# Performance work log

Hardware: AMD Instinct MI355X
Metric: run time of the kernel (lower is better)

Reference implementation:

```python
import jax, jax.numpy as jnp
import numpy as np

CHUNK = 1024  # rows of pc0 processed per tile to avoid materializing the full NxM matrix


def _min_sqdist(a, b):
    """For each row of a [N,3], min squared distance to rows of b [M,3]."""
    b_sq = jnp.sum(b * b, axis=1)  # [M]

    def tile_min(ac):  # ac: [CHUNK, 3]
        d = jnp.sum(ac * ac, axis=1)[:, None] + b_sq[None, :] - 2.0 * (ac @ b.T)
        return jnp.min(d, axis=1)

    n, dim = a.shape
    return jax.lax.map(tile_min, a.reshape(n // CHUNK, CHUNK, dim)).reshape(n)


def setup_inputs() -> dict:
    key = jax.random.key(0)
    k0, k1 = jax.random.split(key)
    pc0 = jax.random.normal(k0, (65536, 3), dtype=jnp.float32)
    pc1 = jax.random.normal(k1, (65536, 3), dtype=jnp.float32)
    return {"pc0": pc0, "pc1": pc1}


def reference(pc0, pc1):
    # chamfer forward: dist0[i] = min_j ||pc0[i]-pc1[j]||^2
    dist0 = _min_sqdist(pc0, pc1)
    mask = dist0 <= 2.0
    # mean over selected elements (boolean mask is constant wrt grads, as in torch)
    return jnp.sum(jnp.where(mask, dist0, 0.0)) / jnp.sum(mask).astype(dist0.dtype)
```

## Files before the change

kernel.cpp:

```cpp
#include <hip/hip_runtime.h>


constexpr int   NPTS  = 65536;
constexpr int   G     = 64;
constexpr int   NC    = G * G * G;
constexpr float H     = 0.125f;
constexpr float ORG   = -4.0f;
constexpr float INVH  = 8.0f;
constexpr int   BLOCK = 256;
constexpr int   PBLOCKS = 256;
constexpr int   SB    = 128;
constexpr int   CHUNK = NC / SB;

__device__ __forceinline__ int cellOf(float x) {
  int c = (int)floorf((x - ORG) * INVH);
  return min(max(c, 0), G - 1);
}

__global__ __launch_bounds__(BLOCK) void count_kernel(
    const float* __restrict__ pc0, const float* __restrict__ pc1,
    unsigned* __restrict__ counts0, unsigned* __restrict__ counts1) {
  const int gid = blockIdx.x * BLOCK + threadIdx.x;
  const float* p; unsigned* cnt; int i;
  if (gid < NPTS) { p = pc1; cnt = counts1; i = gid; }
  else            { p = pc0; cnt = counts0; i = gid - NPTS; }
  const float x = p[3 * i], y = p[3 * i + 1], z = p[3 * i + 2];
  const int cid = (cellOf(z) * G + cellOf(y)) * G + cellOf(x);
  atomicAdd(&cnt[cid], 1u);
}

__global__ __launch_bounds__(1024) void scan_partial_kernel(
    const unsigned* __restrict__ counts0, const unsigned* __restrict__ counts1,
    unsigned* __restrict__ partials) {
  const unsigned* counts = blockIdx.y ? counts0 : counts1;
  const int base = blockIdx.x * CHUNK + threadIdx.x * 2;
  unsigned sum = counts[base] + counts[base + 1];
  for (int o = 32; o; o >>= 1) sum += __shfl_down(sum, o, 64);
  __shared__ unsigned ws[16];
  if ((threadIdx.x & 63) == 0) ws[threadIdx.x >> 6] = sum;
  __syncthreads();
  if (threadIdx.x == 0) {
    unsigned t = 0;
    for (int w = 0; w < 16; ++w) t += ws[w];
    partials[blockIdx.y * SB + blockIdx.x] = t;
  }
}

__global__ __launch_bounds__(256) void scan_mid_kernel(
    unsigned* __restrict__ partials) {
  const int tid = threadIdx.x;
  const int g   = tid >> 7;
  const int li  = tid & 127;
  const unsigned v = partials[g * SB + li];
  unsigned inc = v;
  for (int o = 1; o < 64; o <<= 1) {
    const unsigned t = __shfl_up(inc, o, 64);
    if ((tid & 63) >= o) inc += t;
  }
  __shared__ unsigned wt[4];
  if ((tid & 63) == 63) wt[tid >> 6] = inc;
  __syncthreads();
  const unsigned woff = ((tid >> 6) & 1) ? wt[g << 1] : 0u;
  partials[g * SB + li] = woff + inc - v;
}

__global__ __launch_bounds__(1024) void scan_final_kernel(
    const unsigned* __restrict__ counts0, unsigned* __restrict__ cur0,
    const unsigned* __restrict__ counts1, unsigned* __restrict__ cur1,
    const unsigned* __restrict__ partials) {
  const unsigned* counts = blockIdx.y ? counts0 : counts1;
  unsigned* cur          = blockIdx.y ? cur0    : cur1;
  const int tid = threadIdx.x;
  const int base = blockIdx.x * CHUNK + tid * 2;
  const unsigned a = counts[base], b = counts[base + 1];
  const unsigned tsum = a + b;
  unsigned inc = tsum;
  for (int o = 1; o < 64; o <<= 1) {
    const unsigned t = __shfl_up(inc, o, 64);
    if ((tid & 63) >= o) inc += t;
  }
  __shared__ unsigned wt[16];
  if ((tid & 63) == 63) wt[tid >> 6] = inc;
  __syncthreads();
  if (tid < 16) {
    unsigned w = wt[tid];
    for (int o = 1; o < 16; o <<= 1) {
      const unsigned t = __shfl_up(w, o, 16);
      if (tid >= o) w += t;
    }
    wt[tid] = w;
  }
  __syncthreads();
  const unsigned woff = (tid >> 6) ? wt[(tid >> 6) - 1] : 0u;
  const unsigned off =
      partials[blockIdx.y * SB + blockIdx.x] + woff + inc - tsum;
  cur[base] = off;
  cur[base + 1] = off + a;
}

__global__ __launch_bounds__(BLOCK) void scatter_kernel(
    const float* __restrict__ pc0, const float* __restrict__ pc1,
    unsigned* __restrict__ cur0, unsigned* __restrict__ cur1,
    float4* __restrict__ q, float4* __restrict__ s) {
  const int gid = blockIdx.x * BLOCK + threadIdx.x;
  const float* p; unsigned* cur; float4* dst; int i;
  if (gid < NPTS) { p = pc1; cur = cur1; dst = s; i = gid; }
  else            { p = pc0; cur = cur0; dst = q; i = gid - NPTS; }
  const float x = p[3 * i], y = p[3 * i + 1], z = p[3 * i + 2];
  const int cid = (cellOf(z) * G + cellOf(y)) * G + cellOf(x);
  const unsigned pos = atomicAdd(&cur[cid], 1u);
  dst[pos] = make_float4(x, y, z, 0.f);
}

__global__ __launch_bounds__(BLOCK) void query_kernel(
    const float4* __restrict__ q, const unsigned* __restrict__ ends,
    const float4* __restrict__ s,
    unsigned* __restrict__ wl, float* __restrict__ wlBest,
    unsigned* __restrict__ pendCnt, float* __restrict__ bkt) {
  const int i = blockIdx.x * BLOCK + threadIdx.x;
  const float4 p = q[i];
  const int cx = cellOf(p.x), cy = cellOf(p.y), cz = cellOf(p.z);
  const int x0 = max(cx - 1, 0), x1 = min(cx + 1, G - 1);

  unsigned rs[9], re[9];
#pragma unroll
  for (int rr = 0; rr < 9; ++rr) {
    const int zz = cz + rr / 3 - 1, yy = cy + rr % 3 - 1;
    const bool ok = (zz >= 0) && (zz < G) && (yy >= 0) && (yy < G);
    const int rb = ok ? (zz * G + yy) * G : 0;
    rs[rr] = ok ? ((rb + x0) ? ends[rb + x0 - 1] : 0u) : 0u;
    re[rr] = ok ? ends[rb + x1] : 0u;
  }
  float best = 3.4e38f;
#pragma unroll
  for (int rr = 0; rr < 9; ++rr) {
#pragma unroll 4
    for (unsigned j = rs[rr]; j < re[rr]; ++j) {
      const float4 c = s[j];
      const float dx = p.x - c.x, dy = p.y - c.y, dz = p.z - c.z;
      best = fminf(best, fmaf(dx, dx, fmaf(dy, dy, dz * dz)));
    }
  }

  float v = 0.f, c = 0.f;
  if (best > H * H) {
    const unsigned k = atomicAdd(pendCnt, 1u);
    wl[k] = (unsigned)i; wlBest[k] = best;
  } else if (best <= 2.0f) { v = best; c = 1.0f; }

  for (int o = 32; o; o >>= 1) {
    v += __shfl_down(v, o, 64);
    c += __shfl_down(c, o, 64);
  }
  __shared__ float wsum[BLOCK / 64], wcnt[BLOCK / 64];
  const int wid = threadIdx.x >> 6;
  if ((threadIdx.x & 63) == 0) { wsum[wid] = v; wcnt[wid] = c; }
  __syncthreads();
  if (threadIdx.x == 0) {
    float bv = 0.f, bc = 0.f;
    for (int w = 0; w < BLOCK / 64; ++w) { bv += wsum[w]; bc += wcnt[w]; }
    if (bc != 0.f) {
      atomicAdd(&bkt[2 * (blockIdx.x & 63) + 0], bv);
      atomicAdd(&bkt[2 * (blockIdx.x & 63) + 1], bc);
    }
  }
}

__global__ __launch_bounds__(BLOCK) void pending_kernel(
    const float4* __restrict__ q, const unsigned* __restrict__ ends,
    const float4* __restrict__ s,
    const unsigned* __restrict__ wl, const float* __restrict__ wlBest,
    unsigned* __restrict__ pendCnt, float* __restrict__ bkt,
    unsigned* __restrict__ done, float* __restrict__ out) {
  __shared__ int snP;
  __shared__ float wsum[BLOCK / 64], wcnt[BLOCK / 64];
  __shared__ int isLast;
  __shared__ float fs[BLOCK / 64], fc[BLOCK / 64];
  if (threadIdx.x == 0) snP = (int)atomicAdd(pendCnt, 0u);
  __syncthreads();
  const int lane = threadIdx.x & 63, wid = threadIdx.x >> 6;
  const int gw = blockIdx.x * (BLOCK / 64) + wid;
  const int nW = PBLOCKS * (BLOCK / 64);
  float v = 0.f, c = 0.f;

  for (int it = gw; it < snP; it += nW) {
    const unsigned qi = wl[it];
    const float4 p = q[qi];
    const int cx = cellOf(p.x), cy = cellOf(p.y), cz = cellOf(p.z);
    float best = wlBest[it];

    for (int r = 2; r <= G; ++r) {
      const float cov = H * (float)(r - 1);
      if (best <= cov * cov) break;
      if (best > 2.0f && cov * cov >= 2.0f) break;
      const int S = 8 * r + 2 * (2 * r - 1) * (2 * r - 1);
      float b = best;
      for (int sI = lane; sI < S; sI += 64) {
        int dz, dy, xa, xb;
        if (sI < 8 * r) {
          if (sI < 2 * r + 1)      { dz = -r; dy = sI - r; }
          else if (sI < 4 * r + 2) { dz =  r; dy = sI - (2 * r + 1) - r; }
          else { const int t2 = sI - (4 * r + 2); dz = (t2 >> 1) - (r - 1);
                 dy = (t2 & 1) ? r : -r; }
          xa = cx - r; xb = cx + r;
        } else {
          const int t2 = sI - 8 * r, ci = t2 >> 1, w1 = 2 * r - 1;
          dz = ci / w1 - (r - 1); dy = ci % w1 - (r - 1);
          xa = xb = (t2 & 1) ? cx + r : cx - r;
        }
        const int zz = cz + dz, yy = cy + dy;
        if (zz < 0 || zz >= G || yy < 0 || yy >= G) continue;
        const int a = max(xa, 0), e = min(xb, G - 1);
        if (a > e) continue;
        const int rb = (zz * G + yy) * G;
        const unsigned js = (rb + a) ? ends[rb + a - 1] : 0u;
        const unsigned je = ends[rb + e];
        for (unsigned j = js; j < je; ++j) {
          const float4 cd = s[j];
          const float dx = p.x - cd.x, dyv = p.y - cd.y, dzv = p.z - cd.z;
          b = fminf(b, fmaf(dx, dx, fmaf(dyv, dyv, dzv * dzv)));
        }
      }
      for (int o = 32; o; o >>= 1) b = fminf(b, __shfl_xor(b, o, 64));
      best = b;
    }
    if (lane == 0 && best <= 2.0f) { v += best; c += 1.0f; }
  }

  if (lane == 0) { wsum[wid] = v; wcnt[wid] = c; }
  __syncthreads();
  if (threadIdx.x == 0) {
    float bv = 0.f, bc = 0.f;
    for (int w = 0; w < BLOCK / 64; ++w) { bv += wsum[w]; bc += wcnt[w]; }
    if (bc != 0.f) {
      atomicAdd(&bkt[2 * (blockIdx.x & 63) + 0], bv);
      atomicAdd(&bkt[2 * (blockIdx.x & 63) + 1], bc);
    }
    __threadfence();
    isLast = (atomicAdd(done, 1u) == (unsigned)(PBLOCKS - 1));
  }
  __syncthreads();
  if (isLast) {
    const float val = (threadIdx.x < 128) ? atomicAdd(&bkt[threadIdx.x], 0.0f) : 0.0f;
    float sv = (threadIdx.x & 1) ? 0.f : val;
    float cv = (threadIdx.x & 1) ? val : 0.f;
    for (int o = 32; o; o >>= 1) {
      sv += __shfl_down(sv, o, 64);
      cv += __shfl_down(cv, o, 64);
    }
    if (lane == 0) { fs[wid] = sv; fc[wid] = cv; }
    __syncthreads();
    if (threadIdx.x == 0) {
      float S = 0.f, C = 0.f;
      for (int w = 0; w < BLOCK / 64; ++w) { S += fs[w]; C += fc[w]; }
      out[0] = S / C;
    }
  }
}

extern "C" void kernel_launch(void* const* d_in, const int* in_sizes, int n_in,
                              void* d_out, int out_size, void* d_ws, size_t ws_size,
                              hipStream_t stream) {
  const float* pc0 = (const float*)d_in[0];
  const float* pc1 = (const float*)d_in[1];
  float* out = (float*)d_out;

  char* w = (char*)d_ws;
  auto nxt = [&](size_t bytes) {
    char* p = w; w += (bytes + 255) & ~(size_t)255; return p;
  };
  unsigned* counts1  = (unsigned*)nxt((size_t)NC * 4);
  unsigned* counts0  = (unsigned*)nxt((size_t)NC * 4);
  char*     misc     = nxt(1024);
  float*    bkt      = (float*)misc;
  unsigned* done     = (unsigned*)(misc + 512);
  unsigned* pendCnt  = (unsigned*)(misc + 516);
  unsigned* partials = (unsigned*)nxt((size_t)2 * SB * 4);
  unsigned* cur1     = (unsigned*)nxt((size_t)NC * 4);
  unsigned* cur0     = (unsigned*)nxt((size_t)NC * 4);
  float4*   s        = (float4*)nxt((size_t)NPTS * 16);
  float4*   q        = (float4*)nxt((size_t)NPTS * 16);
  unsigned* wl       = (unsigned*)nxt((size_t)NPTS * 4);
  float*    wlBest   = (float*)nxt((size_t)NPTS * 4);

  hipMemsetAsync(counts1, 0, (size_t)2 * NC * 4 + 1024, stream);

  count_kernel<<<2 * NPTS / BLOCK, BLOCK, 0, stream>>>(pc0, pc1, counts0, counts1);
  scan_partial_kernel<<<dim3(SB, 2), 1024, 0, stream>>>(counts0, counts1, partials);
  scan_mid_kernel<<<1, 256, 0, stream>>>(partials);
  scan_final_kernel<<<dim3(SB, 2), 1024, 0, stream>>>(counts0, cur0,
                                                      counts1, cur1, partials);
  scatter_kernel<<<2 * NPTS / BLOCK, BLOCK, 0, stream>>>(
      pc0, pc1, cur0, cur1, q, s);
  query_kernel<<<NPTS / BLOCK, BLOCK, 0, stream>>>(q, cur1, s, wl, wlBest,
                                                   pendCnt, bkt);
  pending_kernel<<<PBLOCKS, BLOCK, 0, stream>>>(q, cur1, s, wl, wlBest,
                                                pendCnt, bkt, done, out);
}
```

Before: 157.0 us.

## Add coarse 16^3 grid for pending-query ring search

Builds a second, coarser uniform grid (cell size 0.5) over pc1 alongside the fine 64^3 grid. Its counts, prefix scan and scatter are folded into the existing count, scan_mid and scatter kernels. The pending_kernel, which handles queries not resolved by the fine 3x3x3 search, now expands rings over the coarse grid (at most 4 rings) instead of many fine rings. This cuts per-query ring iterations and end-offset lookups for far queries, at the cost of an extra atomic scatter, 1 MB more workspace, and a larger single-block scan.

```diff
diff --git a/kernel.cpp b/kernel.cpp
--- a/kernel.cpp
+++ b/kernel.cpp
@@ -7,6 +7,10 @@
 constexpr float H     = 0.125f;
 constexpr float ORG   = -4.0f;
 constexpr float INVH  = 8.0f;
+constexpr int   G2    = 16;
+constexpr int   NC2   = G2 * G2 * G2;
+constexpr float H2    = 0.5f;
+constexpr float INVH2 = 2.0f;
 constexpr int   BLOCK = 256;
 constexpr int   PBLOCKS = 256;
 constexpr int   SB    = 128;
@@ -16,17 +20,25 @@
   int c = (int)floorf((x - ORG) * INVH);
   return min(max(c, 0), G - 1);
 }
+__device__ __forceinline__ int cellOf2(float x) {
+  int c = (int)floorf((x - ORG) * INVH2);
+  return min(max(c, 0), G2 - 1);
+}
 
 __global__ __launch_bounds__(BLOCK) void count_kernel(
     const float* __restrict__ pc0, const float* __restrict__ pc1,
-    unsigned* __restrict__ counts0, unsigned* __restrict__ counts1) {
+    unsigned* __restrict__ counts0, unsigned* __restrict__ counts1,
+    unsigned* __restrict__ counts2) {
   const int gid = blockIdx.x * BLOCK + threadIdx.x;
-  const float* p; unsigned* cnt; int i;
-  if (gid < NPTS) { p = pc1; cnt = counts1; i = gid; }
-  else            { p = pc0; cnt = counts0; i = gid - NPTS; }
-  const float x = p[3 * i], y = p[3 * i + 1], z = p[3 * i + 2];
-  const int cid = (cellOf(z) * G + cellOf(y)) * G + cellOf(x);
-  atomicAdd(&cnt[cid], 1u);
+  if (gid < NPTS) {
+    const float x = pc1[3 * gid], y = pc1[3 * gid + 1], z = pc1[3 * gid + 2];
+    atomicAdd(&counts1[(cellOf(z) * G + cellOf(y)) * G + cellOf(x)], 1u);
+    atomicAdd(&counts2[(cellOf2(z) * G2 + cellOf2(y)) * G2 + cellOf2(x)], 1u);
+  } else {
+    const int i = gid - NPTS;
+    const float x = pc0[3 * i], y = pc0[3 * i + 1], z = pc0[3 * i + 2];
+    atomicAdd(&counts0[(cellOf(z) * G + cellOf(y)) * G + cellOf(x)], 1u);
+  }
 }
 
 __global__ __launch_bounds__(1024) void scan_partial_kernel(
@@ -46,22 +58,52 @@
   }
 }
 
-__global__ __launch_bounds__(256) void scan_mid_kernel(
-    unsigned* __restrict__ partials) {
+__global__ __launch_bounds__(1024) void scan_mid_kernel(
+    unsigned* __restrict__ partials,
+    const unsigned* __restrict__ counts2, unsigned* __restrict__ cur2) {
+  __shared__ unsigned wt[4];
+  __shared__ unsigned wt2[16];
   const int tid = threadIdx.x;
-  const int g   = tid >> 7;
-  const int li  = tid & 127;
-  const unsigned v = partials[g * SB + li];
-  unsigned inc = v;
+  unsigned v = 0, inc = 0; int g = 0, li = 0;
+  if (tid < 256) {
+    g = tid >> 7; li = tid & 127;
+    v = partials[g * SB + li];
+    inc = v;
+    for (int o = 1; o < 64; o <<= 1) {
+      const unsigned t = __shfl_up(inc, o, 64);
+      if ((tid & 63) >= o) inc += t;
+    }
+    if ((tid & 63) == 63) wt[tid >> 6] = inc;
+  }
+  __syncthreads();
+  if (tid < 256) {
+    const unsigned woff = ((tid >> 6) & 1) ? wt[g << 1] : 0u;
+    partials[g * SB + li] = woff + inc - v;
+  }
+  const int base = tid * 4;
+  const unsigned c0 = counts2[base], c1 = counts2[base + 1],
+                 c2 = counts2[base + 2], c3 = counts2[base + 3];
+  const unsigned run = c0 + c1 + c2 + c3;
+  unsigned inc2 = run;
   for (int o = 1; o < 64; o <<= 1) {
-    const unsigned t = __shfl_up(inc, o, 64);
-    if ((tid & 63) >= o) inc += t;
-  }
-  __shared__ unsigned wt[4];
-  if ((tid & 63) == 63) wt[tid >> 6] = inc;
-  __syncthreads();
-  const unsigned woff = ((tid >> 6) & 1) ? wt[g << 1] : 0u;
-  partials[g * SB + li] = woff + inc - v;
+    const unsigned t = __shfl_up(inc2, o, 64);
+    if ((tid & 63) >= o) inc2 += t;
+  }
+  if ((tid & 63) == 63) wt2[tid >> 6] = inc2;
+  __syncthreads();
+  if (tid < 16) {
+    unsigned w = wt2[tid];
+    for (int o = 1; o < 16; o <<= 1) {
+      const unsigned t = __shfl_up(w, o, 16);
+      if (tid >= o) w += t;
+    }
+    wt2[tid] = w;
+  }
+  __syncthreads();
+  const unsigned woff2 = (tid >> 6) ? wt2[(tid >> 6) - 1] : 0u;
+  unsigned r = woff2 + inc2 - run;
+  cur2[base] = r; cur2[base + 1] = r + c0;
+  cur2[base + 2] = r + c0 + c1; cur2[base + 3] = r + c0 + c1 + c2;
 }
 
 __global__ __launch_bounds__(1024) void scan_final_kernel(
@@ -101,15 +143,22 @@
 __global__ __launch_bounds__(BLOCK) void scatter_kernel(
     const float* __restrict__ pc0, const float* __restrict__ pc1,
     unsigned* __restrict__ cur0, unsigned* __restrict__ cur1,
-    float4* __restrict__ q, float4* __restrict__ s) {
+    unsigned* __restrict__ cur2,
+    float4* __restrict__ q, float4* __restrict__ s, float4* __restrict__ s2) {
   const int gid = blockIdx.x * BLOCK + threadIdx.x;
-  const float* p; unsigned* cur; float4* dst; int i;
-  if (gid < NPTS) { p = pc1; cur = cur1; dst = s; i = gid; }
-  else            { p = pc0; cur = cur0; dst = q; i = gid - NPTS; }
-  const float x = p[3 * i], y = p[3 * i + 1], z = p[3 * i + 2];
-  const int cid = (cellOf(z) * G + cellOf(y)) * G + cellOf(x);
-  const unsigned pos = atomicAdd(&cur[cid], 1u);
-  dst[pos] = make_float4(x, y, z, 0.f);
+  if (gid < NPTS) {
+    const float x = pc1[3 * gid], y = pc1[3 * gid + 1], z = pc1[3 * gid + 2];
+    const float4 pt = make_float4(x, y, z, 0.f);
+    const int cid  = (cellOf(z) * G + cellOf(y)) * G + cellOf(x);
+    const int cid2 = (cellOf2(z) * G2 + cellOf2(y)) * G2 + cellOf2(x);
+    s[atomicAdd(&cur1[cid], 1u)] = pt;
+    s2[atomicAdd(&cur2[cid2], 1u)] = pt;
+  } else {
+    const int i = gid - NPTS;
+    const float x = pc0[3 * i], y = pc0[3 * i + 1], z = pc0[3 * i + 2];
+    const int cid = (cellOf(z) * G + cellOf(y)) * G + cellOf(x);
+    q[atomicAdd(&cur0[cid], 1u)] = make_float4(x, y, z, 0.f);
+  }
 }
 
 __global__ __launch_bounds__(BLOCK) void query_kernel(
@@ -167,8 +216,8 @@
 }
 
 __global__ __launch_bounds__(BLOCK) void pending_kernel(
-    const float4* __restrict__ q, const unsigned* __restrict__ ends,
-    const float4* __restrict__ s,
+    const float4* __restrict__ q,
+    const unsigned* __restrict__ ends2, const float4* __restrict__ s2,
     const unsigned* __restrict__ wl, const float* __restrict__ wlBest,
     unsigned* __restrict__ pendCnt, float* __restrict__ bkt,
     unsigned* __restrict__ done, float* __restrict__ out) {
@@ -186,18 +235,20 @@
   for (int it = gw; it < snP; it += nW) {
     const unsigned qi = wl[it];
     const float4 p = q[qi];
-    const int cx = cellOf(p.x), cy = cellOf(p.y), cz = cellOf(p.z);
+    const int cx = cellOf2(p.x), cy = cellOf2(p.y), cz = cellOf2(p.z);
     float best = wlBest[it];
 
-    for (int r = 2; r <= G; ++r) {
-      const float cov = H * (float)(r - 1);
+    for (int r = 1; r <= 4; ++r) {
+      const float cov = H2 * (float)(r - 1);
       if (best <= cov * cov) break;
       if (best > 2.0f && cov * cov >= 2.0f) break;
-      const int S = 8 * r + 2 * (2 * r - 1) * (2 * r - 1);
+      const int S = (r == 1) ? 9 : 8 * r + 2 * (2 * r - 1) * (2 * r - 1);
       float b = best;
       for (int sI = lane; sI < S; sI += 64) {
         int dz, dy, xa, xb;
-        if (sI < 8 * r) {
+        if (r == 1) {
+          dz = sI / 3 - 1; dy = sI % 3 - 1; xa = cx - 1; xb = cx + 1;
+        } else if (sI < 8 * r) {
           if (sI < 2 * r + 1)      { dz = -r; dy = sI - r; }
           else if (sI < 4 * r + 2) { dz =  r; dy = sI - (2 * r + 1) - r; }
           else { const int t2 = sI - (4 * r + 2); dz = (t2 >> 1) - (r - 1);
@@ -209,14 +260,14 @@
           xa = xb = (t2 & 1) ? cx + r : cx - r;
         }
         const int zz = cz + dz, yy = cy + dy;
-        if (zz < 0 || zz >= G || yy < 0 || yy >= G) continue;
-        const int a = max(xa, 0), e = min(xb, G - 1);
+        if (zz < 0 || zz >= G2 || yy < 0 || yy >= G2) continue;
+        const int a = max(xa, 0), e = min(xb, G2 - 1);
         if (a > e) continue;
-        const int rb = (zz * G + yy) * G;
-        const unsigned js = (rb + a) ? ends[rb + a - 1] : 0u;
-        const unsigned je = ends[rb + e];
+        const int rb = (zz * G2 + yy) * G2;
+        const unsigned js = (rb + a) ? ends2[rb + a - 1] : 0u;
+        const unsigned je = ends2[rb + e];
         for (unsigned j = js; j < je; ++j) {
-          const float4 cd = s[j];
+          const float4 cd = s2[j];
           const float dx = p.x - cd.x, dyv = p.y - cd.y, dzv = p.z - cd.z;
           b = fminf(b, fmaf(dx, dx, fmaf(dyv, dyv, dzv * dzv)));
         }
@@ -271,6 +322,7 @@
   };
   unsigned* counts1  = (unsigned*)nxt((size_t)NC * 4);
   unsigned* counts0  = (unsigned*)nxt((size_t)NC * 4);
+  unsigned* counts2  = (unsigned*)nxt((size_t)NC2 * 4);
   char*     misc     = nxt(1024);
   float*    bkt      = (float*)misc;
   unsigned* done     = (unsigned*)(misc + 512);
@@ -278,22 +330,25 @@
   unsigned* partials = (unsigned*)nxt((size_t)2 * SB * 4);
   unsigned* cur1     = (unsigned*)nxt((size_t)NC * 4);
   unsigned* cur0     = (unsigned*)nxt((size_t)NC * 4);
+  unsigned* cur2     = (unsigned*)nxt((size_t)NC2 * 4);
   float4*   s        = (float4*)nxt((size_t)NPTS * 16);
+  float4*   s2       = (float4*)nxt((size_t)NPTS * 16);
   float4*   q        = (float4*)nxt((size_t)NPTS * 16);
   unsigned* wl       = (unsigned*)nxt((size_t)NPTS * 4);
   float*    wlBest   = (float*)nxt((size_t)NPTS * 4);
 
-  hipMemsetAsync(counts1, 0, (size_t)2 * NC * 4 + 1024, stream);
-
-  count_kernel<<<2 * NPTS / BLOCK, BLOCK, 0, stream>>>(pc0, pc1, counts0, counts1);
+  hipMemsetAsync(counts1, 0, (size_t)2 * NC * 4 + (size_t)NC2 * 4 + 1024, stream);
+
+  count_kernel<<<2 * NPTS / BLOCK, BLOCK, 0, stream>>>(pc0, pc1,
+                                                       counts0, counts1, counts2);
   scan_partial_kernel<<<dim3(SB, 2), 1024, 0, stream>>>(counts0, counts1, partials);
-  scan_mid_kernel<<<1, 256, 0, stream>>>(partials);
+  scan_mid_kernel<<<1, 1024, 0, stream>>>(partials, counts2, cur2);
   scan_final_kernel<<<dim3(SB, 2), 1024, 0, stream>>>(counts0, cur0,
                                                       counts1, cur1, partials);
   scatter_kernel<<<2 * NPTS / BLOCK, BLOCK, 0, stream>>>(
-      pc0, pc1, cur0, cur1, q, s);
+      pc0, pc1, cur0, cur1, cur2, q, s, s2);
   query_kernel<<<NPTS / BLOCK, BLOCK, 0, stream>>>(q, cur1, s, wl, wlBest,
                                                    pendCnt, bkt);
-  pending_kernel<<<PBLOCKS, BLOCK, 0, stream>>>(q, cur1, s, wl, wlBest,
+  pending_kernel<<<PBLOCKS, BLOCK, 0, stream>>>(q, cur2, s2, wl, wlBest,
                                                 pendCnt, bkt, done, out);
 }
```

Measured after the change: 311.1 us. 98.1% more time.

## Split query scan across thread pairs and use coarser shells in pending search

Applied to the files above, without the earlier changes.

The query kernel now gives two threads to each query point. Each thread scans alternating candidates in the 3x3x3 neighbourhood, and the pair merges its minimum with a lane shuffle, which doubles the thread count to spread the per-point work. The pending kernel now expands shells over a coarser 32^3 virtual grid built from 2x2 blocks of fine cells. This needs fewer shell iterations and wave reductions per far point, but scans more candidates per shell. Halving useful lanes in the reduction path and the coarser shells may cost extra work in exchange.

```diff
diff --git a/kernel.cpp b/kernel.cpp
--- a/kernel.cpp
+++ b/kernel.cpp
@@ -7,6 +7,9 @@
 constexpr float H     = 0.125f;
 constexpr float ORG   = -4.0f;
 constexpr float INVH  = 8.0f;
+constexpr int   G3    = 32;
+constexpr float H3    = 0.25f;
+constexpr float INVH3 = 4.0f;
 constexpr int   BLOCK = 256;
 constexpr int   PBLOCKS = 256;
 constexpr int   SB    = 128;
@@ -15,6 +18,10 @@
 __device__ __forceinline__ int cellOf(float x) {
   int c = (int)floorf((x - ORG) * INVH);
   return min(max(c, 0), G - 1);
+}
+__device__ __forceinline__ int cellOf3(float x) {
+  int c = (int)floorf((x - ORG) * INVH3);
+  return min(max(c, 0), G3 - 1);
 }
 
 __global__ __launch_bounds__(BLOCK) void count_kernel(
@@ -25,8 +32,7 @@
   if (gid < NPTS) { p = pc1; cnt = counts1; i = gid; }
   else            { p = pc0; cnt = counts0; i = gid - NPTS; }
   const float x = p[3 * i], y = p[3 * i + 1], z = p[3 * i + 2];
-  const int cid = (cellOf(z) * G + cellOf(y)) * G + cellOf(x);
-  atomicAdd(&cnt[cid], 1u);
+  atomicAdd(&cnt[(cellOf(z) * G + cellOf(y)) * G + cellOf(x)], 1u);
 }
 
 __global__ __launch_bounds__(1024) void scan_partial_kernel(
@@ -108,8 +114,7 @@
   else            { p = pc0; cur = cur0; dst = q; i = gid - NPTS; }
   const float x = p[3 * i], y = p[3 * i + 1], z = p[3 * i + 2];
   const int cid = (cellOf(z) * G + cellOf(y)) * G + cellOf(x);
-  const unsigned pos = atomicAdd(&cur[cid], 1u);
-  dst[pos] = make_float4(x, y, z, 0.f);
+  dst[atomicAdd(&cur[cid], 1u)] = make_float4(x, y, z, 0.f);
 }
 
 __global__ __launch_bounds__(BLOCK) void query_kernel(
@@ -117,7 +122,9 @@
     const float4* __restrict__ s,
     unsigned* __restrict__ wl, float* __restrict__ wlBest,
     unsigned* __restrict__ pendCnt, float* __restrict__ bkt) {
-  const int i = blockIdx.x * BLOCK + threadIdx.x;
+  const int gtid = blockIdx.x * BLOCK + threadIdx.x;
+  const int i   = gtid >> 1;
+  const int sub = gtid & 1;
   const float4 p = q[i];
   const int cx = cellOf(p.x), cy = cellOf(p.y), cz = cellOf(p.z);
   const int x0 = max(cx - 1, 0), x1 = min(cx + 1, G - 1);
@@ -135,18 +142,21 @@
 #pragma unroll
   for (int rr = 0; rr < 9; ++rr) {
 #pragma unroll 4
-    for (unsigned j = rs[rr]; j < re[rr]; ++j) {
+    for (unsigned j = rs[rr] + sub; j < re[rr]; j += 2) {
       const float4 c = s[j];
       const float dx = p.x - c.x, dy = p.y - c.y, dz = p.z - c.z;
       best = fminf(best, fmaf(dx, dx, fmaf(dy, dy, dz * dz)));
     }
   }
+  best = fminf(best, __shfl_xor(best, 1, 64));
 
   float v = 0.f, c = 0.f;
-  if (best > H * H) {
-    const unsigned k = atomicAdd(pendCnt, 1u);
-    wl[k] = (unsigned)i; wlBest[k] = best;
-  } else if (best <= 2.0f) { v = best; c = 1.0f; }
+  if (sub == 0) {
+    if (best > H * H) {
+      const unsigned k = atomicAdd(pendCnt, 1u);
+      wl[k] = (unsigned)i; wlBest[k] = best;
+    } else if (best <= 2.0f) { v = best; c = 1.0f; }
+  }
 
   for (int o = 32; o; o >>= 1) {
     v += __shfl_down(v, o, 64);
@@ -167,8 +177,8 @@
 }
 
 __global__ __launch_bounds__(BLOCK) void pending_kernel(
-    const float4* __restrict__ q, const unsigned* __restrict__ ends,
-    const float4* __restrict__ s,
+    const float4* __restrict__ q,
+    const unsigned* __restrict__ ends, const float4* __restrict__ s,
     const unsigned* __restrict__ wl, const float* __restrict__ wlBest,
     unsigned* __restrict__ pendCnt, float* __restrict__ bkt,
     unsigned* __restrict__ done, float* __restrict__ out) {
@@ -186,18 +196,20 @@
   for (int it = gw; it < snP; it += nW) {
     const unsigned qi = wl[it];
     const float4 p = q[qi];
-    const int cx = cellOf(p.x), cy = cellOf(p.y), cz = cellOf(p.z);
+    const int cx = cellOf3(p.x), cy = cellOf3(p.y), cz = cellOf3(p.z);
     float best = wlBest[it];
 
-    for (int r = 2; r <= G; ++r) {
-      const float cov = H * (float)(r - 1);
+    for (int r = 1; r <= 8; ++r) {
+      const float cov = H3 * (float)(r - 1);
       if (best <= cov * cov) break;
       if (best > 2.0f && cov * cov >= 2.0f) break;
-      const int S = 8 * r + 2 * (2 * r - 1) * (2 * r - 1);
+      const int S = (r == 1) ? 9 : 8 * r + 2 * (2 * r - 1) * (2 * r - 1);
       float b = best;
       for (int sI = lane; sI < S; sI += 64) {
         int dz, dy, xa, xb;
-        if (sI < 8 * r) {
+        if (r == 1) {
+          dz = sI / 3 - 1; dy = sI % 3 - 1; xa = cx - 1; xb = cx + 1;
+        } else if (sI < 8 * r) {
           if (sI < 2 * r + 1)      { dz = -r; dy = sI - r; }
           else if (sI < 4 * r + 2) { dz =  r; dy = sI - (2 * r + 1) - r; }
           else { const int t2 = sI - (4 * r + 2); dz = (t2 >> 1) - (r - 1);
@@ -208,17 +220,26 @@
           dz = ci / w1 - (r - 1); dy = ci % w1 - (r - 1);
           xa = xb = (t2 & 1) ? cx + r : cx - r;
         }
-        const int zz = cz + dz, yy = cy + dy;
-        if (zz < 0 || zz >= G || yy < 0 || yy >= G) continue;
-        const int a = max(xa, 0), e = min(xb, G - 1);
-        if (a > e) continue;
-        const int rb = (zz * G + yy) * G;
-        const unsigned js = (rb + a) ? ends[rb + a - 1] : 0u;
-        const unsigned je = ends[rb + e];
-        for (unsigned j = js; j < je; ++j) {
-          const float4 cd = s[j];
-          const float dx = p.x - cd.x, dyv = p.y - cd.y, dzv = p.z - cd.z;
-          b = fminf(b, fmaf(dx, dx, fmaf(dyv, dyv, dzv * dzv)));
+        const int Z = cz + dz, Y = cy + dy;
+        if (Z < 0 || Z >= G3 || Y < 0 || Y >= G3) continue;
+        const int a3 = max(xa, 0), e3 = min(xb, G3 - 1);
+        if (a3 > e3) continue;
+        const int xs = 2 * a3, xe = 2 * e3 + 1;
+        unsigned js[4], je[4];
+#pragma unroll
+        for (int k = 0; k < 4; ++k) {
+          const int zz = 2 * Z + (k >> 1), yy = 2 * Y + (k & 1);
+          const int rb = (zz * G + yy) * G;
+          js[k] = (rb + xs) ? ends[rb + xs - 1] : 0u;
+          je[k] = ends[rb + xe];
+        }
+#pragma unroll
+        for (int k = 0; k < 4; ++k) {
+          for (unsigned j = js[k]; j < je[k]; ++j) {
+            const float4 cd = s[j];
+            const float dx = p.x - cd.x, dyv = p.y - cd.y, dzv = p.z - cd.z;
+            b = fminf(b, fmaf(dx, dx, fmaf(dyv, dyv, dzv * dzv)));
+          }
         }
       }
       for (int o = 32; o; o >>= 1) b = fminf(b, __shfl_xor(b, o, 64));
@@ -292,8 +313,8 @@
                                                       counts1, cur1, partials);
   scatter_kernel<<<2 * NPTS / BLOCK, BLOCK, 0, stream>>>(
       pc0, pc1, cur0, cur1, q, s);
-  query_kernel<<<NPTS / BLOCK, BLOCK, 0, stream>>>(q, cur1, s, wl, wlBest,
-                                                   pendCnt, bkt);
+  query_kernel<<<2 * NPTS / BLOCK, BLOCK, 0, stream>>>(q, cur1, s, wl, wlBest,
+                                                       pendCnt, bkt);
   pending_kernel<<<PBLOCKS, BLOCK, 0, stream>>>(q, cur1, s, wl, wlBest,
                                                 pendCnt, bkt, done, out);
 }
```

Result: faster. 151.8 us (median of 2 runs) (-3.4%).
